# Kernel optimization log

Measured on AMD Instinct MI355X. Metric: run time of the kernel, lower is better.

## Reference

```python
import jax, jax.numpy as jnp
import numpy as np
from jax import lax

N_EMBD = 1024
N_HEAD = 16
HEAD_DIM = N_EMBD // N_HEAD
EPS = 1e-6
B, T = 4, 2048


def setup_inputs() -> dict:
    key = jax.random.key(0)
    ks = jax.random.split(key, 5)
    scale = 1.0 / np.sqrt(N_EMBD)
    return {
        "x": jax.random.normal(ks[0], (B, T, N_EMBD), jnp.float32),
        "W_attn": jax.random.normal(ks[1], (N_EMBD, 3 * N_EMBD), jnp.float32) * scale,
        "b_attn": jax.random.normal(ks[2], (3 * N_EMBD,), jnp.float32) * 0.01,
        "W_proj": jax.random.normal(ks[3], (N_EMBD, N_EMBD), jnp.float32) * scale,
        "b_proj": jax.random.normal(ks[4], (N_EMBD,), jnp.float32) * 0.01,
    }


def _feature_map(x):
    # ELU + 1 for non-negativity
    return jax.nn.elu(x) + 1.0


def reference(x, W_attn, b_attn, W_proj, b_proj):
    Bb, Tt, C = x.shape
    qkv = x @ W_attn + b_attn  # (B,T,3C)
    q, k, v = jnp.split(qkv, 3, axis=-1)

    def to_heads(t):
        # (B,T,C) -> (T,B,H,d): scan axis leading
        return t.reshape(Bb, Tt, N_HEAD, HEAD_DIM).transpose(1, 0, 2, 3)

    q = _feature_map(to_heads(q))
    k = _feature_map(to_heads(k))
    v = to_heads(v)

    # Causal linear attention: O(d^2) running state instead of the torch
    # code's materialized (B,H,T,d,d) cumsum — same math.
    def step(carry, inp):
        kv, ksum = carry  # (B,H,d,d), (B,H,d)
        qt, kt, vt = inp  # each (B,H,d)
        kv = kv + kt[..., :, None] * vt[..., None, :]
        ksum = ksum + kt
        num = jnp.einsum('bhi,bhij->bhj', qt, kv)
        den = jnp.einsum('bhi,bhi->bh', qt, ksum)[..., None] + EPS
        return (kv, ksum), num / den

    init = (
        jnp.zeros((Bb, N_HEAD, HEAD_DIM, HEAD_DIM), x.dtype),
        jnp.zeros((Bb, N_HEAD, HEAD_DIM), x.dtype),
    )
    _, y = lax.scan(step, init, (q, k, v))  # (T,B,H,d)
    y = y.transpose(1, 0, 2, 3).reshape(Bb, Tt, C)
    return y @ W_proj + b_proj  # dropout is identity in eval mode
```

## Files before the change

kernel.cpp:

```cpp
#include <hip/hip_runtime.h>
#include <math.h>

#define BB   4
#define TT   2048
#define CC   1024
#define HH   16
#define DD   64
#define MM   (BB*TT)
#define NQKV (3*CC)
#define LCH  128
#define NCH  (TT/LCH)
#define EPSF 1e-6f

#define QKST 72
#define PST  136
#define VTST 136

typedef __bf16 bf16x8 __attribute__((ext_vector_type(8)));
typedef float  floatx4 __attribute__((ext_vector_type(4)));

__device__ __forceinline__ unsigned short f2bf(float f) {
  union { float f; unsigned int u; } v; v.f = f;
  unsigned int r = v.u + 0x7fffu + ((v.u >> 16) & 1u);
  return (unsigned short)(r >> 16);
}
__device__ __forceinline__ float bf2f(unsigned short s) {
  union { unsigned int u; float f; } v; v.u = ((unsigned int)s) << 16;
  return v.f;
}
__device__ __forceinline__ float featmap(float v) {
  return v > 0.f ? v + 1.f : __expf(v);
}
__device__ __forceinline__ void gld_lds_b128(const unsigned short* g, unsigned short* l) {
  __builtin_amdgcn_global_load_lds(
      (const __attribute__((address_space(1))) unsigned int*)g,
      (__attribute__((address_space(3))) unsigned int*)l, 16, 0, 0);
}

__device__ __forceinline__ void transpose_cvt_body(const float* __restrict__ W,
                                                   unsigned short* __restrict__ out,
                                                   int R, int Cc, int bx32, int by32, int tid) {
  __shared__ float tile[32][33];
  int tx = tid & 31, ty = tid >> 5;
  int bx = bx32 * 32, by = by32 * 32;
  #pragma unroll
  for (int i = ty; i < 32; i += 8)
    tile[i][tx] = W[(size_t)(by + i) * Cc + bx + tx];
  __syncthreads();
  #pragma unroll
  for (int i = ty; i < 32; i += 8)
    out[(size_t)(bx + i) * R + by + tx] = f2bf(tile[tx][i]);
}

__global__ __launch_bounds__(256) void prep_kernel(
    const float* __restrict__ x, unsigned short* __restrict__ xb,
    const float* __restrict__ Wa, unsigned short* __restrict__ WaT,
    const float* __restrict__ Wp, unsigned short* __restrict__ WpT) {
  int blk = blockIdx.x, tid = threadIdx.x;
  if (blk < 8192) {
    int i = (blk * 256 + tid) * 4;
    float4 f = *(const float4*)(x + i);
    ushort4 o;
    o.x = f2bf(f.x); o.y = f2bf(f.y); o.z = f2bf(f.z); o.w = f2bf(f.w);
    *(ushort4*)(xb + i) = o;
  } else if (blk < 8192 + 3072) {
    int t = blk - 8192;
    transpose_cvt_body(Wa, WaT, CC, NQKV, t % 96, t / 96, tid);
  } else {
    int t = blk - 11264;
    transpose_cvt_body(Wp, WpT, CC, CC, t % 32, t / 32, tid);
  }
}

#define GEMM_K_LOOP(A_, Bt_, K_)                                                 \
  __shared__ __align__(16) unsigned short As[128 * 64];                          \
  __shared__ __align__(16) unsigned short Bs[128 * 64];                          \
  int tid = threadIdx.x;                                                         \
  int wave = tid >> 6, lane = tid & 63;                                          \
  int lr = lane & 15, lq = lane >> 4;                                            \
  int m0 = blockIdx.y * 128, n0 = blockIdx.x * 128;                              \
  int wm = (wave >> 1) * 64, wn = (wave & 1) * 64;                               \
  int lrow = lane >> 3;                        \
  int lk = (lane & 7) ^ lrow;                       \
  int rbase = wave * 32;                                                         \
  const unsigned short* gA = A_ + (size_t)(m0 + rbase + lrow) * K_ + lk * 8;     \
  const unsigned short* gB = Bt_ + (size_t)(n0 + rbase + lrow) * K_ + lk * 8;    \
  unsigned short* lA = As + rbase * 64;                                          \
  unsigned short* lB = Bs + rbase * 64;                                          \
  floatx4 acc[4][4] = {};                                                        \
  for (int k0 = 0; k0 < K_; k0 += 64) {                                          \
    __syncthreads();                 \
    _Pragma("unroll")                                                            \
    for (int g = 0; g < 4; g++) {                                                \
      gld_lds_b128(gA + k0 + (size_t)g * 8 * K_, lA + g * 512);                  \
      gld_lds_b128(gB + k0 + (size_t)g * 8 * K_, lB + g * 512);                  \
    }                                                                            \
    __syncthreads();                                    \
    _Pragma("unroll")                                                            \
    for (int kk = 0; kk < 2; kk++) {                                             \
      bf16x8 an[4], bm[4];                                                       \
      _Pragma("unroll")                                                          \
      for (int i = 0; i < 4; i++)                                                \
        an[i] = *(const bf16x8*)&Bs[(wn + i * 16 + lr) * 64 + ((((kk << 2) + lq) ^ (lr & 7)) << 3)]; \
      _Pragma("unroll")                                                          \
      for (int j = 0; j < 4; j++)                                                \
        bm[j] = *(const bf16x8*)&As[(wm + j * 16 + lr) * 64 + ((((kk << 2) + lq) ^ (lr & 7)) << 3)]; \
      _Pragma("unroll")                                                          \
      for (int i = 0; i < 4; i++)                                                \
        _Pragma("unroll")                                                        \
        for (int j = 0; j < 4; j++)                                              \
          acc[i][j] = __builtin_amdgcn_mfma_f32_16x16x32_bf16(an[i], bm[j], acc[i][j], 0, 0, 0); \
    }                                                                            \
  }

#define BKQ   32
#define ASLT  (256 * BKQ)
#define BSLT  (192 * BKQ)
#define NT_Q  (CC / BKQ)

__global__ __launch_bounds__(512, 2) void gemm_qkv_kernel(
    const unsigned short* __restrict__ A, const unsigned short* __restrict__ Bt,
    const float* __restrict__ bias,
    unsigned short* __restrict__ qh, unsigned short* __restrict__ kh,
    unsigned short* __restrict__ vh) {
  extern __shared__ __align__(16) unsigned short lds[];
  unsigned short* Ar = lds;
  unsigned short* Br = lds + 4 * ASLT;

  const int tid = threadIdx.x;
  const int wave = tid >> 6, lane = tid & 63;
  const int lr = lane & 15, lq = lane >> 4;
  const int m0 = blockIdx.y * 256, n0 = blockIdx.x * 192;
  const int wm = (wave >> 2) * 128, wn = (wave & 3) * 48;

  const int srow = wave * 16 + (lane >> 2);
  const int cs = (lane & 3) ^ ((lane >> 3) & 3);
  const unsigned short* gA0 = A  + (size_t)(m0 + srow) * CC + cs * 8;
  const unsigned short* gB0 = Bt + (size_t)(n0 + srow) * CC + cs * 8;
  unsigned short* const stA = Ar + wave * 512;
  unsigned short* const stB = Br + wave * 512;
  const bool bhi = (wave < 4);

  const int chunk = lq ^ ((lr >> 1) & 3);
  const int roA = (wm + lr) * BKQ + chunk * 8;
  const int roB = (wn + lr) * BKQ + chunk * 8;

  floatx4 acc[3][8] = {};

#define QSTAGE_A(tt) do {                                      \
    const unsigned short* g_ = gA0 + (tt) * BKQ;               \
    unsigned short* d_ = stA + ((tt) & 3) * ASLT;              \
    gld_lds_b128(g_, d_);                                      \
    gld_lds_b128(g_ + (size_t)128 * CC, d_ + 4096);            \
  } while (0)
#define QSTAGE_B(tt) do {                                      \
    const unsigned short* g_ = gB0 + (tt) * BKQ;               \
    unsigned short* d_ = stB + ((tt) & 3) * BSLT;              \
    gld_lds_b128(g_, d_);                                      \
    if (bhi) gld_lds_b128(g_ + (size_t)128 * CC, d_ + 4096);   \
  } while (0)

  QSTAGE_A(0); QSTAGE_B(0);
  QSTAGE_A(1); QSTAGE_B(1);
  QSTAGE_A(2); QSTAGE_B(2);
  asm volatile("s_waitcnt vmcnt(6)" ::: "memory");
  __builtin_amdgcn_s_barrier();

  #pragma unroll 4
  for (int t = 0; t < NT_Q; ++t) {
    const unsigned short* sA = Ar + (t & 3) * ASLT + roA;
    const unsigned short* sB = Br + (t & 3) * BSLT + roB;
    bf16x8 an[3], bm[4], bm2[4];
    #pragma unroll
    for (int i = 0; i < 3; i++) an[i] = *(const bf16x8*)(sB + i * (16 * BKQ));
    #pragma unroll
    for (int j = 0; j < 4; j++) bm[j] = *(const bf16x8*)(sA + j * (16 * BKQ));
    if (t < NT_Q - 3) QSTAGE_A(t + 3);
    __builtin_amdgcn_s_barrier();
    asm volatile("s_waitcnt lgkmcnt(0)" ::: "memory");
    __builtin_amdgcn_s_setprio(1);
    #pragma unroll
    for (int i = 0; i < 3; i++)
      #pragma unroll
      for (int j = 0; j < 4; j++)
        acc[i][j] = __builtin_amdgcn_mfma_f32_16x16x32_bf16(an[i], bm[j], acc[i][j], 0, 0, 0);
    __builtin_amdgcn_s_setprio(0);
    __builtin_amdgcn_s_barrier();
    #pragma unroll
    for (int j = 0; j < 4; j++) bm2[j] = *(const bf16x8*)(sA + (4 + j) * (16 * BKQ));
    if (t < NT_Q - 3) QSTAGE_B(t + 3);
    __builtin_amdgcn_s_barrier();
    asm volatile("s_waitcnt lgkmcnt(0)" ::: "memory");
    __builtin_amdgcn_s_setprio(1);
    #pragma unroll
    for (int i = 0; i < 3; i++)
      #pragma unroll
      for (int j = 0; j < 4; j++)
        acc[i][4 + j] = __builtin_amdgcn_mfma_f32_16x16x32_bf16(an[i], bm2[j], acc[i][4 + j], 0, 0, 0);
    __builtin_amdgcn_s_setprio(0);
    if (t < NT_Q - 3)        asm volatile("s_waitcnt vmcnt(6)" ::: "memory");
    else if (t == NT_Q - 3)  asm volatile("s_waitcnt vmcnt(3)" ::: "memory");
    else if (t == NT_Q - 2)  asm volatile("s_waitcnt vmcnt(0)" ::: "memory");
    __builtin_amdgcn_s_barrier();
  }
#undef QSTAGE_A
#undef QSTAGE_B

  unsigned short* dstv[3];
  size_t qoff[3];
  float4 bi[3];
  bool feat[3];
  #pragma unroll
  for (int i = 0; i < 3; i++) {
    const int n = n0 + wn + i * 16 + lq * 4;
    dstv[i] = (n < 1024) ? qh : (n < 2048) ? kh : vh;
    feat[i] = (n < 2048);
    const int h = (n & 1023) >> 6, dd = n & 63;
    qoff[i] = (size_t)h * (TT * DD) + dd;
    bi[i] = *(const float4*)&bias[n];
  }
  #pragma unroll
  for (int j = 0; j < 8; j++) {
    const int m = m0 + wm + j * 16 + lr;
    const int b = m >> 11, tg = m & 2047;
    const size_t pj = (size_t)b * (HH * TT * DD) + (size_t)tg * DD;
    #pragma unroll
    for (int i = 0; i < 3; i++) {
      float v0 = acc[i][j][0] + bi[i].x, v1 = acc[i][j][1] + bi[i].y;
      float v2 = acc[i][j][2] + bi[i].z, v3 = acc[i][j][3] + bi[i].w;
      if (feat[i]) { v0 = featmap(v0); v1 = featmap(v1); v2 = featmap(v2); v3 = featmap(v3); }
      ushort4 o; o.x = f2bf(v0); o.y = f2bf(v1); o.z = f2bf(v2); o.w = f2bf(v3);
      *(ushort4*)&dstv[i][pj + qoff[i]] = o;
    }
  }
}

__global__ __launch_bounds__(256) void gemm_proj_kernel(
    const unsigned short* __restrict__ A, const unsigned short* __restrict__ Bt,
    const float* __restrict__ bias, float* __restrict__ out) {
  GEMM_K_LOOP(A, Bt, CC)
  #pragma unroll
  for (int i = 0; i < 4; i++) {
    int n = n0 + wn + i * 16 + lq * 4;
    float4 bi = *(const float4*)&bias[n];
    #pragma unroll
    for (int j = 0; j < 4; j++) {
      int m = m0 + wm + j * 16 + lr;
      float4 o;
      o.x = acc[i][j][0] + bi.x; o.y = acc[i][j][1] + bi.y;
      o.z = acc[i][j][2] + bi.z; o.w = acc[i][j][3] + bi.w;
      *(float4*)&out[(size_t)m * CC + n] = o;
    }
  }
}

__global__ __launch_bounds__(256) void chunk_state_kernel(
    const unsigned short* __restrict__ kh, const unsigned short* __restrict__ vh,
    float* __restrict__ KVx) {
  __shared__ __align__(16) unsigned short Kt[64 * VTST];
  __shared__ __align__(16) unsigned short Vt[80 * VTST];
  int blk = blockIdx.x;
  int bh = blk / NCH, c = blk % NCH;
  int tid = threadIdx.x;
  const unsigned short* kp = kh + ((size_t)bh * TT + c * LCH) * DD;
  const unsigned short* vp = vh + ((size_t)bh * TT + c * LCH) * DD;
  {
    int t = tid & 127;
    for (int j8 = (tid >> 7) * 8; j8 < DD; j8 += 16) {
      union { uint4 u; unsigned short s[8]; } wk, wv;
      wk.u = *(const uint4*)&kp[(size_t)t * DD + j8];
      wv.u = *(const uint4*)&vp[(size_t)t * DD + j8];
      #pragma unroll
      for (int jj = 0; jj < 8; jj++) {
        Kt[(j8 + jj) * VTST + t] = wk.s[jj];
        Vt[(j8 + jj) * VTST + t] = wv.s[jj];
      }
    }
  }
  for (int e = tid; e < 16 * 128; e += 256) {
    int rr = e >> 7, n = e & 127;
    Vt[(64 + rr) * VTST + n] = (rr == 0) ? (unsigned short)0x3F80 : (unsigned short)0;
  }
  __syncthreads();
  int wave = tid >> 6, lane = tid & 63;
  int lr = lane & 15, lq = lane >> 4;
  int i0 = wave * 16;
  floatx4 acc[5] = {};
  #pragma unroll
  for (int kk = 0; kk < 4; kk++) {
    bf16x8 a = *(const bf16x8*)&Kt[(i0 + lr) * VTST + kk * 32 + lq * 8];
    #pragma unroll
    for (int jt = 0; jt < 5; jt++) {
      bf16x8 b = *(const bf16x8*)&Vt[(jt * 16 + lr) * VTST + kk * 32 + lq * 8];
      acc[jt] = __builtin_amdgcn_mfma_f32_16x16x32_bf16(a, b, acc[jt], 0, 0, 0);
    }
  }
  float* o = KVx + (size_t)blk * 5120;
  #pragma unroll
  for (int jt = 0; jt < 5; jt++)
    *(float4*)&o[(jt * 16 + lr) * 64 + i0 + lq * 4] = *(float4*)&acc[jt];
}

__global__ __launch_bounds__(256) void prefix_state_kernel(const float* __restrict__ KVx,
                                                           unsigned short* __restrict__ SPb) {
  int bh = blockIdx.x / 5, jb = blockIdx.x % 5;
  int e = jb * 1024 + threadIdx.x * 4;
  float run0 = 0.f, run1 = 0.f, run2 = 0.f, run3 = 0.f;
  for (int c = 0; c < NCH; c++) {
    size_t base = ((size_t)bh * NCH + c) * 5120 + e;
    float4 v = *(const float4*)&KVx[base];
    ushort4 o;
    o.x = f2bf(run0); o.y = f2bf(run1); o.z = f2bf(run2); o.w = f2bf(run3);
    *(ushort4*)&SPb[base] = o;
    run0 += v.x; run1 += v.y; run2 += v.z; run3 += v.w;
  }
}

__global__ __launch_bounds__(256) void chunk_attn_kernel(
    const unsigned short* __restrict__ qh, const unsigned short* __restrict__ kh,
    const unsigned short* __restrict__ vh, const unsigned short* __restrict__ SPb,
    unsigned short* __restrict__ yb) {
  __shared__ __align__(16) unsigned short lds[128 * QKST * 2 + 80 * VTST];
  unsigned short* Qs = lds;
  unsigned short* Ks = lds + 128 * QKST;
  unsigned short* P  = lds;
  unsigned short* Vt = lds + 128 * QKST * 2;

  int blk = blockIdx.x;
  int bh = blk / NCH, c = blk % NCH;
  int b = bh / HH, h = bh % HH;
  int tid = threadIdx.x;
  const unsigned short* qp = qh + ((size_t)bh * TT + c * LCH) * DD;
  const unsigned short* kp = kh + ((size_t)bh * TT + c * LCH) * DD;
  const unsigned short* vp = vh + ((size_t)bh * TT + c * LCH) * DD;

  for (int e = tid; e < 1024; e += 256) {
    int row = e >> 3, k8 = (e & 7) * 8;
    *(uint4*)&Qs[row * QKST + k8] = *(const uint4*)&qp[(size_t)row * DD + k8];
    *(uint4*)&Ks[row * QKST + k8] = *(const uint4*)&kp[(size_t)row * DD + k8];
  }
  {
    int t = tid & 127;
    for (int j8 = (tid >> 7) * 8; j8 < DD; j8 += 16) {
      union { uint4 u; unsigned short s[8]; } w;
      w.u = *(const uint4*)&vp[(size_t)t * DD + j8];
      #pragma unroll
      for (int jj = 0; jj < 8; jj++) Vt[(j8 + jj) * VTST + t] = w.s[jj];
    }
  }
  for (int e = tid; e < 16 * 128; e += 256) {
    int rr = e >> 7, n = e & 127;
    Vt[(64 + rr) * VTST + n] = (rr == 0) ? (unsigned short)0x3F80 : (unsigned short)0;
  }
  __syncthreads();

  int wave = tid >> 6, lane = tid & 63;
  int lr = lane & 15, lq = lane >> 4;
  int mbase = wave * 32;

  bf16x8 aq[2][2];
  #pragma unroll
  for (int i = 0; i < 2; i++)
    #pragma unroll
    for (int kk = 0; kk < 2; kk++)
      aq[i][kk] = *(const bf16x8*)&Qs[(mbase + i * 16 + lr) * QKST + kk * 32 + lq * 8];

  floatx4 accT[5][2] = {};
  const unsigned short* spb = SPb + (size_t)blk * (80 * 64);
  __builtin_amdgcn_s_setprio(1);
  #pragma unroll
  for (int jt = 0; jt < 5; jt++)
    #pragma unroll
    for (int kk = 0; kk < 2; kk++) {
      bf16x8 asp = *(const bf16x8*)&spb[(jt * 16 + lr) * 64 + kk * 32 + lq * 8];
      accT[jt][0] = __builtin_amdgcn_mfma_f32_16x16x32_bf16(asp, aq[0][kk], accT[jt][0], 0, 0, 0);
      accT[jt][1] = __builtin_amdgcn_mfma_f32_16x16x32_bf16(asp, aq[1][kk], accT[jt][1], 0, 0, 0);
    }
  __builtin_amdgcn_s_setprio(0);
  floatx4 sacc[2][8] = {};
  __builtin_amdgcn_s_setprio(1);
  #pragma unroll
  for (int nt = 0; nt < 8; nt++)
    #pragma unroll
    for (int kk = 0; kk < 2; kk++) {
      bf16x8 bk = *(const bf16x8*)&Ks[(nt * 16 + lr) * QKST + kk * 32 + lq * 8];
      sacc[0][nt] = __builtin_amdgcn_mfma_f32_16x16x32_bf16(aq[0][kk], bk, sacc[0][nt], 0, 0, 0);
      sacc[1][nt] = __builtin_amdgcn_mfma_f32_16x16x32_bf16(aq[1][kk], bk, sacc[1][nt], 0, 0, 0);
    }
  __builtin_amdgcn_s_setprio(0);
  __syncthreads();

  #pragma unroll
  for (int i = 0; i < 2; i++)
    #pragma unroll
    for (int nt = 0; nt < 8; nt++) {
      int col = nt * 16 + lr;
      #pragma unroll
      for (int r = 0; r < 4; r++) {
        int m = mbase + i * 16 + lq * 4 + r;
        float v = (col <= m) ? sacc[i][nt][r] : 0.f;
        P[m * PST + col] = f2bf(v);
      }
    }
  __syncthreads();

  #pragma unroll
  for (int kk4 = 0; kk4 < 4; kk4++) {
    bf16x8 bp0 = *(const bf16x8*)&P[(mbase + lr) * PST + kk4 * 32 + lq * 8];
    bf16x8 bp1 = *(const bf16x8*)&P[(mbase + 16 + lr) * PST + kk4 * 32 + lq * 8];
    __builtin_amdgcn_s_setprio(1);
    #pragma unroll
    for (int jt = 0; jt < 5; jt++) {
      bf16x8 av = *(const bf16x8*)&Vt[(jt * 16 + lr) * VTST + kk4 * 32 + lq * 8];
      accT[jt][0] = __builtin_amdgcn_mfma_f32_16x16x32_bf16(av, bp0, accT[jt][0], 0, 0, 0);
      accT[jt][1] = __builtin_amdgcn_mfma_f32_16x16x32_bf16(av, bp1, accT[jt][1], 0, 0, 0);
    }
    __builtin_amdgcn_s_setprio(0);
  }

  #pragma unroll
  for (int it = 0; it < 2; it++) {
    float den = __shfl(accT[4][it][0], lr, 64);
    float inv = 1.f / (den + EPSF);
    int tg = c * LCH + mbase + it * 16 + lr;
    size_t base = ((size_t)b * TT + tg) * CC + h * DD;
    #pragma unroll
    for (int jt = 0; jt < 4; jt++) {
      ushort4 o;
      o.x = f2bf(accT[jt][it][0] * inv);
      o.y = f2bf(accT[jt][it][1] * inv);
      o.z = f2bf(accT[jt][it][2] * inv);
      o.w = f2bf(accT[jt][it][3] * inv);
      *(ushort4*)&yb[base + jt * 16 + lq * 4] = o;
    }
  }
}

extern "C" void kernel_launch(void* const* d_in, const int* in_sizes, int n_in,
                              void* d_out, int out_size, void* d_ws, size_t ws_size,
                              hipStream_t stream) {
  const float* x      = (const float*)d_in[0];
  const float* W_attn = (const float*)d_in[1];
  const float* b_attn = (const float*)d_in[2];
  const float* W_proj = (const float*)d_in[3];
  const float* b_proj = (const float*)d_in[4];
  float* out = (float*)d_out;

  char* ws = (char*)d_ws;
  size_t off = 0;
  auto alloc = [&](size_t bytes) -> char* {
    char* p = ws + off;
    off += (bytes + 255) & ~(size_t)255;
    return p;
  };
  unsigned short* xb  = (unsigned short*)alloc((size_t)MM * CC * 2);
  unsigned short* WaT = (unsigned short*)alloc((size_t)NQKV * CC * 2);
  unsigned short* WpT = (unsigned short*)alloc((size_t)CC * CC * 2);
  unsigned short* qh  = (unsigned short*)alloc((size_t)MM * CC * 2);
  unsigned short* kh  = (unsigned short*)alloc((size_t)MM * CC * 2);
  unsigned short* vh  = (unsigned short*)alloc((size_t)MM * CC * 2);
  float* KVx = (float*)alloc((size_t)BB * HH * NCH * 80 * 64 * 4);
  unsigned short* SPb = (unsigned short*)alloc((size_t)BB * HH * NCH * 80 * 64 * 2);
  unsigned short* yb = xb;

  static bool s_attr_done = false;
  if (!s_attr_done) {
    (void)hipFuncSetAttribute((const void*)gemm_qkv_kernel,
                              hipFuncAttributeMaxDynamicSharedMemorySize, 114688);
    s_attr_done = true;
  }

  prep_kernel<<<12288, 256, 0, stream>>>(x, xb, W_attn, WaT, W_proj, WpT);
  gemm_qkv_kernel<<<dim3(NQKV / 192, MM / 256), 512, 114688, stream>>>(xb, WaT, b_attn, qh, kh, vh);
  chunk_state_kernel<<<BB * HH * NCH, 256, 0, stream>>>(kh, vh, KVx);
  prefix_state_kernel<<<BB * HH * 5, 256, 0, stream>>>(KVx, SPb);
  chunk_attn_kernel<<<BB * HH * NCH, 256, 0, stream>>>(qh, kh, vh, SPb, yb);
  gemm_proj_kernel<<<dim3(CC / 128, MM / 128), 256, 0, stream>>>(yb, WpT, b_proj, out);
}
```

Baseline: 235.8 us.

## Merge QKV GEMM half-steps, batch prefix-state loads, drop setprio in chunk attention

The QKV GEMM main loop now loads all eight B fragments at once and issues both A and B stage prefetches together. That removes the split half-iteration and two barriers per K step, at the cost of more live registers. The prefix-state kernel loads all chunk values up front so the loads overlap instead of running one per serial step. The setprio hints around MFMA sections in the chunk attention kernel are removed.

```diff
diff --git a/kernel.cpp b/kernel.cpp
--- a/kernel.cpp
+++ b/kernel.cpp
@@ -170,33 +170,20 @@
   for (int t = 0; t < NT_Q; ++t) {
     const unsigned short* sA = Ar + (t & 3) * ASLT + roA;
     const unsigned short* sB = Br + (t & 3) * BSLT + roB;
-    bf16x8 an[3], bm[4], bm2[4];
+    bf16x8 an[3], bm[8];
     #pragma unroll
     for (int i = 0; i < 3; i++) an[i] = *(const bf16x8*)(sB + i * (16 * BKQ));
     #pragma unroll
-    for (int j = 0; j < 4; j++) bm[j] = *(const bf16x8*)(sA + j * (16 * BKQ));
-    if (t < NT_Q - 3) QSTAGE_A(t + 3);
+    for (int j = 0; j < 8; j++) bm[j] = *(const bf16x8*)(sA + j * (16 * BKQ));
+    if (t < NT_Q - 3) { QSTAGE_A(t + 3); QSTAGE_B(t + 3); }
     __builtin_amdgcn_s_barrier();
     asm volatile("s_waitcnt lgkmcnt(0)" ::: "memory");
     __builtin_amdgcn_s_setprio(1);
     #pragma unroll
     for (int i = 0; i < 3; i++)
       #pragma unroll
-      for (int j = 0; j < 4; j++)
+      for (int j = 0; j < 8; j++)
         acc[i][j] = __builtin_amdgcn_mfma_f32_16x16x32_bf16(an[i], bm[j], acc[i][j], 0, 0, 0);
-    __builtin_amdgcn_s_setprio(0);
-    __builtin_amdgcn_s_barrier();
-    #pragma unroll
-    for (int j = 0; j < 4; j++) bm2[j] = *(const bf16x8*)(sA + (4 + j) * (16 * BKQ));
-    if (t < NT_Q - 3) QSTAGE_B(t + 3);
-    __builtin_amdgcn_s_barrier();
-    asm volatile("s_waitcnt lgkmcnt(0)" ::: "memory");
-    __builtin_amdgcn_s_setprio(1);
-    #pragma unroll
-    for (int i = 0; i < 3; i++)
-      #pragma unroll
-      for (int j = 0; j < 4; j++)
-        acc[i][4 + j] = __builtin_amdgcn_mfma_f32_16x16x32_bf16(an[i], bm2[j], acc[i][4 + j], 0, 0, 0);
     __builtin_amdgcn_s_setprio(0);
     if (t < NT_Q - 3)        asm volatile("s_waitcnt vmcnt(6)" ::: "memory");
     else if (t == NT_Q - 3)  asm volatile("s_waitcnt vmcnt(3)" ::: "memory");
@@ -305,14 +292,18 @@
                                                            unsigned short* __restrict__ SPb) {
   int bh = blockIdx.x / 5, jb = blockIdx.x % 5;
   int e = jb * 1024 + threadIdx.x * 4;
-  float run0 = 0.f, run1 = 0.f, run2 = 0.f, run3 = 0.f;
+  size_t base0 = ((size_t)bh * NCH) * 5120 + e;
+  float4 v[NCH];
+  #pragma unroll
+  for (int c = 0; c < NCH; c++)
+    v[c] = *(const float4*)&KVx[base0 + (size_t)c * 5120];
+  float r0 = 0.f, r1 = 0.f, r2 = 0.f, r3 = 0.f;
+  #pragma unroll
   for (int c = 0; c < NCH; c++) {
-    size_t base = ((size_t)bh * NCH + c) * 5120 + e;
-    float4 v = *(const float4*)&KVx[base];
     ushort4 o;
-    o.x = f2bf(run0); o.y = f2bf(run1); o.z = f2bf(run2); o.w = f2bf(run3);
-    *(ushort4*)&SPb[base] = o;
-    run0 += v.x; run1 += v.y; run2 += v.z; run3 += v.w;
+    o.x = f2bf(r0); o.y = f2bf(r1); o.z = f2bf(r2); o.w = f2bf(r3);
+    *(ushort4*)&SPb[base0 + (size_t)c * 5120] = o;
+    r0 += v[c].x; r1 += v[c].y; r2 += v[c].z; r3 += v[c].w;
   }
 }
 
@@ -367,7 +358,6 @@
 
   floatx4 accT[5][2] = {};
   const unsigned short* spb = SPb + (size_t)blk * (80 * 64);
-  __builtin_amdgcn_s_setprio(1);
   #pragma unroll
   for (int jt = 0; jt < 5; jt++)
     #pragma unroll
@@ -376,9 +366,7 @@
       accT[jt][0] = __builtin_amdgcn_mfma_f32_16x16x32_bf16(asp, aq[0][kk], accT[jt][0], 0, 0, 0);
       accT[jt][1] = __builtin_amdgcn_mfma_f32_16x16x32_bf16(asp, aq[1][kk], accT[jt][1], 0, 0, 0);
     }
-  __builtin_amdgcn_s_setprio(0);
   floatx4 sacc[2][8] = {};
-  __builtin_amdgcn_s_setprio(1);
   #pragma unroll
   for (int nt = 0; nt < 8; nt++)
     #pragma unroll
@@ -387,7 +375,6 @@
       sacc[0][nt] = __builtin_amdgcn_mfma_f32_16x16x32_bf16(aq[0][kk], bk, sacc[0][nt], 0, 0, 0);
       sacc[1][nt] = __builtin_amdgcn_mfma_f32_16x16x32_bf16(aq[1][kk], bk, sacc[1][nt], 0, 0, 0);
     }
-  __builtin_amdgcn_s_setprio(0);
   __syncthreads();
 
   #pragma unroll
@@ -408,14 +395,12 @@
   for (int kk4 = 0; kk4 < 4; kk4++) {
     bf16x8 bp0 = *(const bf16x8*)&P[(mbase + lr) * PST + kk4 * 32 + lq * 8];
     bf16x8 bp1 = *(const bf16x8*)&P[(mbase + 16 + lr) * PST + kk4 * 32 + lq * 8];
-    __builtin_amdgcn_s_setprio(1);
     #pragma unroll
     for (int jt = 0; jt < 5; jt++) {
       bf16x8 av = *(const bf16x8*)&Vt[(jt * 16 + lr) * VTST + kk4 * 32 + lq * 8];
       accT[jt][0] = __builtin_amdgcn_mfma_f32_16x16x32_bf16(av, bp0, accT[jt][0], 0, 0, 0);
       accT[jt][1] = __builtin_amdgcn_mfma_f32_16x16x32_bf16(av, bp1, accT[jt][1], 0, 0, 0);
     }
-    __builtin_amdgcn_s_setprio(0);
   }
 
   #pragma unroll
```

After: 229.6 us. 1.03x faster.
